# Optimization experiments

Hardware: AMD Instinct MI355X
Metric: run time of the kernel (lower is better)

## Reference

```python
import jax, jax.numpy as jnp
import numpy as np

B, T, D, H = 2, 512, 512, 8
HD = D // H
FF = 4 * D
MOM_BETA, NOV_BETA, NOV_GAIN = 0.9, 0.95, 3.0
LR_MIN, LR_MAX, MAX_FW_NORM = 0.5, 3.0, 32.0


def setup_inputs() -> dict:
    key = jax.random.key(0)
    ks = jax.random.split(key, 10)
    s = 1.0 / np.sqrt(D)
    return {
        'x': jax.random.normal(ks[0], (B, T, D), jnp.float32),
        'Wq': jax.random.normal(ks[1], (D, D), jnp.float32) * s,
        'Wk1': jax.random.normal(ks[2], (D, D), jnp.float32) * s,
        'Wk2': jax.random.normal(ks[3], (D, D), jnp.float32) * s,
        'Wv': jax.random.normal(ks[4], (D, D), jnp.float32) * s,
        'Wo': jax.random.normal(ks[5], (D, D), jnp.float32) * s,
        'lambda_logit': jnp.zeros((H,), jnp.float32),  # sigmoid -> lambda_init = 0.5
        'ln1_g': jnp.ones((D,), jnp.float32), 'ln1_b': jnp.zeros((D,), jnp.float32),
        'base_weight': jax.random.normal(ks[6], (D, D), jnp.float32) * s,  # ~xavier
        'ttt_bias': jnp.zeros((D,), jnp.float32),
        'log_inner_lr': jnp.log(jnp.asarray(0.05, jnp.float32)),
        'ln2_g': jnp.ones((D,), jnp.float32), 'ln2_b': jnp.zeros((D,), jnp.float32),
        'W1': jax.random.normal(ks[7], (FF, D), jnp.float32) * s,
        'b1': jnp.zeros((FF,), jnp.float32),
        'W2': jax.random.normal(ks[8], (D, FF), jnp.float32) * (1.0 / np.sqrt(FF)),
        'b2': jnp.zeros((D,), jnp.float32),
        'ln3_g': jnp.ones((D,), jnp.float32), 'ln3_b': jnp.zeros((D,), jnp.float32),
    }


def _ln(x, g, b):
    m = x.mean(-1, keepdims=True)
    v = jnp.mean((x - m) ** 2, -1, keepdims=True)
    return (x - m) / jnp.sqrt(v + 1e-5) * g + b


def _diff_attn(x, Wq, Wk1, Wk2, Wv, Wo, lambda_logit):
    b, t, d = x.shape
    def heads(w):
        return jnp.einsum('btd,od->bto', x, w).reshape(b, t, H, HD).transpose(0, 2, 1, 3)
    q, k1, k2, v = heads(Wq), heads(Wk1), heads(Wk2), heads(Wv)
    scale = HD ** -0.5
    s1 = jnp.einsum('bhqd,bhkd->bhqk', q, k1) * scale
    s2 = jnp.einsum('bhqd,bhkd->bhqk', q, k2) * scale
    mask = jnp.tril(jnp.ones((t, t), bool))
    neg = jnp.finfo(s1.dtype).min
    s1 = jnp.where(mask, s1, neg)
    s2 = jnp.where(mask, s2, neg)
    lam = jax.nn.sigmoid(lambda_logit)[None, :, None, None]
    attn = jax.nn.softmax(s1, -1) - lam * jax.nn.softmax(s2, -1)
    attn = attn / jnp.clip(jnp.abs(attn).sum(-1, keepdims=True), 1e-6, None)
    o = jnp.einsum('bhqk,bhkd->bhqd', attn, v).transpose(0, 2, 1, 3).reshape(b, t, d)
    return jnp.einsum('btd,od->bto', o, Wo)


def _ttt(x, base_weight, ttt_bias, log_inner_lr):
    b = x.shape[0]
    inner_lr = jnp.clip(jnp.exp(log_inner_lr), 1e-5, 1.0)
    fw0 = jnp.broadcast_to(base_weight, (b, D, D)).astype(x.dtype) + 0.0
    mom0 = jnp.zeros_like(fw0)
    ema0 = jnp.zeros((b, D), x.dtype)
    lrm0 = jnp.ones((b, 1), x.dtype)

    def step(carry, x_t):  # x_t: [B, D]
        fw, mom, ema, lrm = carry
        y = jnp.einsum('bij,bj->bi', fw, x_t) + ttt_bias
        err = (y - x_t) / float(D)  # targets=None -> target is x_t
        g = jax.lax.stop_gradient(err[:, :, None] * x_t[:, None, :])  # first_order
        mom2 = MOM_BETA * mom + (1.0 - MOM_BETA) * g
        nov = jnp.abs(x_t - ema).mean(-1, keepdims=True)  # [B, 1]
        lr_scale = jnp.clip(1.0 + NOV_GAIN * nov, LR_MIN, LR_MAX)
        lrm2 = NOV_BETA * lrm + (1.0 - NOV_BETA) * lr_scale
        ema2 = NOV_BETA * ema + (1.0 - NOV_BETA) * x_t
        fw2 = fw - (inner_lr * lrm2)[:, :, None] * mom2
        norm = jnp.clip(jnp.sqrt((fw2 * fw2).sum((1, 2), keepdims=True)), 1e-6, None)
        fw2 = fw2 * jnp.minimum(MAX_FW_NORM / norm, 1.0)
        return (fw2, mom2, ema2, lrm2), y

    _, ys = jax.lax.scan(step, (fw0, mom0, ema0, lrm0), x.transpose(1, 0, 2))
    return ys.transpose(1, 0, 2)


def reference(x, Wq, Wk1, Wk2, Wv, Wo, lambda_logit, ln1_g, ln1_b, base_weight, ttt_bias, log_inner_lr, ln2_g, ln2_b, W1, b1, W2, b2, ln3_g, ln3_b):
    h = x + _diff_attn(_ln(x, ln1_g, ln1_b), Wq, Wk1, Wk2, Wv, Wo, lambda_logit)
    h = h + _ttt(_ln(h, ln2_g, ln2_b), base_weight, ttt_bias, log_inner_lr)
    z = _ln(h, ln3_g, ln3_b)
    z = jax.nn.gelu(jnp.einsum('btd,fd->btf', z, W1) + b1, approximate=False)
    h = h + jnp.einsum('btf,df->btd', z, W2) + b2
    return h
```

## Files before the change

### kernel.cpp

```cpp
#include <hip/hip_runtime.h>
#include <hip/hip_fp16.h>

typedef _Float16 f16;
typedef f16 f16x4 __attribute__((ext_vector_type(4)));
typedef f16 f16x8 __attribute__((ext_vector_type(8)));
typedef float f32x4 __attribute__((ext_vector_type(4)));
typedef unsigned uint2v __attribute__((ext_vector_type(2)));

#define DEVI static __device__ __forceinline__

DEVI void gload_lds16(const void* g, void* l) {
  __builtin_amdgcn_global_load_lds(
      (const __attribute__((address_space(1))) unsigned int*)g,
      (__attribute__((address_space(3))) unsigned int*)l, 16, 0, 0);
}

DEVI float wave_red_sum64(float v) {
#pragma unroll
  for (int m = 1; m < 64; m <<= 1) v += __shfl_xor(v, m, 64);
  return v;
}
DEVI float wave_red_max64(float v) {
#pragma unroll
  for (int m = 1; m < 64; m <<= 1) v = fmaxf(v, __shfl_xor(v, m, 64));
  return v;
}

template <int CTRL>
DEVI float dpp_addf(float v) {
  int s = __builtin_amdgcn_update_dpp(0, __float_as_int(v), CTRL, 0xF, 0xF, true);
  return v + __int_as_float(s);
}
DEVI float xor16_add(float v) {
#if __has_builtin(__builtin_amdgcn_permlane16_swap)
  uint2v r = __builtin_amdgcn_permlane16_swap(__float_as_uint(v), __float_as_uint(v), false, false);
  return __uint_as_float(r.x) + __uint_as_float(r.y);
#else
  int s = __builtin_amdgcn_ds_swizzle(__float_as_int(v), 0x401F);
  return v + __int_as_float(s);
#endif
}
DEVI float xor32_add(float v) {
#if __has_builtin(__builtin_amdgcn_permlane32_swap)
  uint2v r = __builtin_amdgcn_permlane32_swap(__float_as_uint(v), __float_as_uint(v), false, false);
  return __uint_as_float(r.x) + __uint_as_float(r.y);
#else
  int s = __builtin_amdgcn_ds_bpermute(((threadIdx.x & 63) ^ 32) << 2, __float_as_int(v));
  return v + __int_as_float(s);
#endif
}
DEVI float allred64(float v) {
  v = dpp_addf<0xB1>(v);
  v = dpp_addf<0x4E>(v);
  v = dpp_addf<0x141>(v);
  v = dpp_addf<0x140>(v);
  v = xor16_add(v);
  return xor32_add(v);
}
DEVI float red16g(float v) {
  v = dpp_addf<0xB1>(v);
  v = dpp_addf<0x4E>(v);
  v = dpp_addf<0x141>(v);
  v = dpp_addf<0x140>(v);
  return v;
}

__global__ void cvt_all_kernel(const float* __restrict__ s0, const float* __restrict__ s1,
                               const float* __restrict__ s2, const float* __restrict__ s3,
                               const float* __restrict__ s4, const float* __restrict__ s5,
                               const float* __restrict__ s6, f16* __restrict__ d) {
  const int blk = blockIdx.x;
  const float* s; long dofs; int local;
  if (blk < 256)       { s = s0; dofs = 0;       local = blk; }
  else if (blk < 512)  { s = s1; dofs = 262144;  local = blk - 256; }
  else if (blk < 768)  { s = s2; dofs = 524288;  local = blk - 512; }
  else if (blk < 1024) { s = s3; dofs = 786432;  local = blk - 768; }
  else if (blk < 1280) { s = s4; dofs = 1048576; local = blk - 1024; }
  else if (blk < 2304) { s = s5; dofs = 1310720; local = blk - 1280; }
  else                 { s = s6; dofs = 2359296; local = blk - 2304; }
  const long i = (long)local * 1024 + threadIdx.x * 4;
  float4 v = *(const float4*)(s + i);
  f16x4 o = {(f16)v.x, (f16)v.y, (f16)v.z, (f16)v.w};
  *(f16x4*)(d + dofs + i) = o;
}

__global__ void ln_kernel(const float* __restrict__ in, const float* __restrict__ add,
                          const float* __restrict__ g, const float* __restrict__ b,
                          float* __restrict__ sumout, float* __restrict__ lnf,
                          f16* __restrict__ lnh) {
  const int row = blockIdx.x * 4 + (threadIdx.x >> 6);
  const int lane = threadIdx.x & 63;
  const long base = (long)row * 512;
  const int c0 = lane * 4, c1 = 256 + lane * 4;
  float4 a0 = *(const float4*)(in + base + c0);
  float4 a1 = *(const float4*)(in + base + c1);
  if (add) {
    float4 d0 = *(const float4*)(add + base + c0);
    float4 d1 = *(const float4*)(add + base + c1);
    a0.x += d0.x; a0.y += d0.y; a0.z += d0.z; a0.w += d0.w;
    a1.x += d1.x; a1.y += d1.y; a1.z += d1.z; a1.w += d1.w;
  }
  if (sumout) {
    *(float4*)(sumout + base + c0) = a0;
    *(float4*)(sumout + base + c1) = a1;
  }
  float v[8] = {a0.x, a0.y, a0.z, a0.w, a1.x, a1.y, a1.z, a1.w};
  float s = 0.f;
#pragma unroll
  for (int k = 0; k < 8; k++) s += v[k];
  s = wave_red_sum64(s);
  const float mean = s * (1.f / 512.f);
  float vs = 0.f;
#pragma unroll
  for (int k = 0; k < 8; k++) { float d = v[k] - mean; vs += d * d; }
  vs = wave_red_sum64(vs);
  const float rstd = rsqrtf(vs * (1.f / 512.f) + 1e-5f);
  float4 g0 = *(const float4*)(g + c0), g1 = *(const float4*)(g + c1);
  float4 p0 = *(const float4*)(b + c0), p1 = *(const float4*)(b + c1);
  const float gg[8] = {g0.x, g0.y, g0.z, g0.w, g1.x, g1.y, g1.z, g1.w};
  const float bv[8] = {p0.x, p0.y, p0.z, p0.w, p1.x, p1.y, p1.z, p1.w};
  float y[8];
#pragma unroll
  for (int k = 0; k < 8; k++) y[k] = (v[k] - mean) * rstd * gg[k] + bv[k];
  if (lnf) {
    float4 o0 = {y[0], y[1], y[2], y[3]}, o1 = {y[4], y[5], y[6], y[7]};
    *(float4*)(lnf + base + c0) = o0;
    *(float4*)(lnf + base + c1) = o1;
  }
  if (lnh) {
    f16x4 o0 = {(f16)y[0], (f16)y[1], (f16)y[2], (f16)y[3]};
    f16x4 o1 = {(f16)y[4], (f16)y[5], (f16)y[6], (f16)y[7]};
    *(f16x4*)(lnh + base + c0) = o0;
    *(f16x4*)(lnh + base + c1) = o1;
  }
}

enum { EPI_QKV = 0, EPI_SCORES = 2, EPI_PV = 3, EPI_WO = 4, EPI_GELU = 5, EPI_OUT = 6 };

template <int EPI>
__launch_bounds__(256, 1) __global__
void gemm_bt(const f16* __restrict__ A, const f16* __restrict__ W, int lda, int ldw,
             long Az, long Wz, void* __restrict__ dst, const float* __restrict__ bias,
             const float* __restrict__ resid, int K, float scale, int zofs, int hcp) {
  if (EPI == EPI_SCORES && blockIdx.x > blockIdx.y) return;
  __shared__ f16 lA[128 * 64];
  __shared__ f16 lB[128 * 64];
  const int tid = threadIdx.x;
  const int wave = tid >> 6, lane = tid & 63;
  const int z = blockIdx.z;
  const f16* Ab;
  const f16* Wb;
  if (EPI == EPI_SCORES) {
    const int v_ = (z >= hcp) ? 1 : 0, head = z - v_ * hcp;
    Ab = A + (long)head * 32768 + (long)blockIdx.y * 128 * lda;
    Wb = W + (long)v_ * 524288 + (long)head * 32768 + (long)blockIdx.x * 128 * ldw;
  } else {
    Ab = A + (long)z * Az + (long)blockIdx.y * 128 * lda;
    Wb = W + (long)z * Wz + (long)blockIdx.x * 128 * ldw;
  }

  f32x4 acc[4][4];
#pragma unroll
  for (int a = 0; a < 4; a++)
#pragma unroll
    for (int q = 0; q < 4; q++) acc[a][q] = (f32x4){0.f, 0.f, 0.f, 0.f};

  int srow[4], scol[4];
#pragma unroll
  for (int i = 0; i < 4; i++) {
    int c = i * 256 + tid;
    int row = c >> 3;
    int colb = (c & 7) << 4;
    srow[i] = row;
    scol[i] = (colb ^ ((row & 7) << 4)) >> 1;
  }

  for (int k0 = 0; k0 < K; k0 += 64) {
    __syncthreads();
#pragma unroll
    for (int i = 0; i < 4; i++) {
      const int le = (i * 256 + wave * 64) * 8;
      gload_lds16(Ab + (long)srow[i] * lda + k0 + scol[i], lA + le);
      gload_lds16(Wb + (long)srow[i] * ldw + k0 + scol[i], lB + le);
    }
    __syncthreads();
    const int wm = (wave >> 1) * 64, wn = (wave & 1) * 64;
#pragma unroll
    for (int km = 0; km < 2; km++) {
      const int kb = km * 64 + ((lane >> 4) << 4);
      f16x8 af[4], bfv[4];
#pragma unroll
      for (int mf = 0; mf < 4; mf++) {
        int r = wm + mf * 16 + (lane & 15);
        af[mf] = *(const f16x8*)((const char*)lA + r * 128 + (kb ^ ((r & 7) << 4)));
      }
#pragma unroll
      for (int nf = 0; nf < 4; nf++) {
        int r = wn + nf * 16 + (lane & 15);
        bfv[nf] = *(const f16x8*)((const char*)lB + r * 128 + (kb ^ ((r & 7) << 4)));
      }
#pragma unroll
      for (int mf = 0; mf < 4; mf++)
#pragma unroll
        for (int nf = 0; nf < 4; nf++)
          acc[mf][nf] = __builtin_amdgcn_mfma_f32_16x16x32_f16(af[mf], bfv[nf], acc[mf][nf], 0, 0, 0);
    }
  }

  const int wm = (wave >> 1) * 64, wn = (wave & 1) * 64;
  const int rbase = blockIdx.y * 128 + wm + ((lane >> 4) << 2);
  const int cbase = blockIdx.x * 128 + wn + (lane & 15);
#pragma unroll
  for (int mf = 0; mf < 4; mf++)
#pragma unroll
    for (int nf = 0; nf < 4; nf++)
#pragma unroll
      for (int j = 0; j < 4; j++) {
        const int m = rbase + mf * 16 + j;
        const int n = cbase + nf * 16;
        const float v = acc[mf][nf][j];
        if (EPI == EPI_QKV) {
          f16* d = (f16*)dst + (long)z * 524288;
          if (z < 3)
            d[(long)((m >> 9) * 8 + (n >> 6)) * 32768 + (m & 511) * 64 + (n & 63)] = (f16)v;
          else
            d[(long)((m >> 9) * 8 + (n >> 6)) * 32768 + (n & 63) * 512 + (m & 511)] = (f16)v;
        } else if (EPI == EPI_SCORES) {
          ((float*)dst)[(long)z * 262144 + (long)m * 512 + n] = v * scale;
        } else if (EPI == EPI_PV) {
          if (n < 64) {
            const int hh = z + zofs;
            ((f16*)dst)[(long)((hh >> 3) * 512 + m) * 512 + (hh & 7) * 64 + n] = (f16)v;
          }
        } else if (EPI == EPI_WO) {
          ((float*)dst)[(long)m * 512 + n] = v + resid[(long)m * 512 + n];
        } else if (EPI == EPI_GELU) {
          const float u = v + bias[n];
          ((f16*)dst)[(long)m * 2048 + n] = (f16)(0.5f * u * (1.f + erff(u * 0.70710678118f)));
        } else {
          ((float*)dst)[(long)m * 512 + n] = v + bias[n] + resid[(long)m * 512 + n];
        }
      }
}

__global__ void softmax_diff_kernel(const float* __restrict__ S1, const float* __restrict__ S2,
                                    const float* __restrict__ lamlog, f16* __restrict__ attn,
                                    int zofs) {
  const int rid = blockIdx.x * 4 + (threadIdx.x >> 6);
  const int lane = threadIdx.x & 63;
  const int z = rid >> 9, i = rid & 511;
  const float lam = 1.f / (1.f + __expf(-lamlog[(z + zofs) & 7]));
  const long base = (long)z * 262144 + (long)i * 512;
  const int c0 = lane * 4, c1 = 256 + lane * 4;
  float4 xa = *(const float4*)(S1 + base + c0);
  float4 xb = *(const float4*)(S1 + base + c1);
  float4 ya = *(const float4*)(S2 + base + c0);
  float4 yb = *(const float4*)(S2 + base + c1);
  float s1v[8] = {xa.x, xa.y, xa.z, xa.w, xb.x, xb.y, xb.z, xb.w};
  float s2v[8] = {ya.x, ya.y, ya.z, ya.w, yb.x, yb.y, yb.z, yb.w};
  int cols[8];
#pragma unroll
  for (int k = 0; k < 8; k++) cols[k] = (k < 4) ? (c0 + k) : (c1 + k - 4);
  float m1 = -3.0e38f, m2 = -3.0e38f;
#pragma unroll
  for (int k = 0; k < 8; k++)
    if (cols[k] <= i) { m1 = fmaxf(m1, s1v[k]); m2 = fmaxf(m2, s2v[k]); }
  m1 = wave_red_max64(m1);
  m2 = wave_red_max64(m2);
  float z1 = 0.f, z2 = 0.f, e1[8], e2[8];
#pragma unroll
  for (int k = 0; k < 8; k++) {
    const bool valid = cols[k] <= i;
    e1[k] = valid ? __expf(s1v[k] - m1) : 0.f;
    e2[k] = valid ? __expf(s2v[k] - m2) : 0.f;
    z1 += e1[k]; z2 += e2[k];
  }
  z1 = wave_red_sum64(z1);
  z2 = wave_red_sum64(z2);
  const float r1 = 1.f / z1, r2 = lam / z2;
  float p[8], l1 = 0.f;
#pragma unroll
  for (int k = 0; k < 8; k++) { p[k] = e1[k] * r1 - e2[k] * r2; l1 += fabsf(p[k]); }
  l1 = wave_red_sum64(l1);
  const float rn = 1.f / fmaxf(l1, 1e-6f);
  f16x4 o0 = {(f16)(p[0] * rn), (f16)(p[1] * rn), (f16)(p[2] * rn), (f16)(p[3] * rn)};
  f16x4 o1 = {(f16)(p[4] * rn), (f16)(p[5] * rn), (f16)(p[6] * rn), (f16)(p[7] * rn)};
  *(f16x4*)(attn + base + c0) = o0;
  *(f16x4*)(attn + base + c1) = o1;
}

#define ALD4(dst, p) asm volatile("global_load_dwordx4 %0, %1, off" : "=&v"(dst) : "v"(p) : "memory")
#define ALD1(dst, p) asm volatile("global_load_dword %0, %1, off" : "=&v"(dst) : "v"(p) : "memory")
#define VMWAIT(N)                                                             \
  {                                                                           \
    asm volatile("s_waitcnt vmcnt(" #N ")" ::: "memory");                     \
    __builtin_amdgcn_sched_barrier(0);                                        \
  }

#define EISSUE(X)                                                             \
  {                                                                           \
    ALD1(X[0], pe);        ALD1(X[1], pe + 512);                              \
    ALD1(X[2], pe + 1024); ALD1(X[3], pe + 1536);                             \
    ALD1(X[4], pe + 2048); ALD1(X[5], pe + 2560);                             \
    ALD1(X[6], pe + 3072); ALD1(X[7], pe + 3584);                             \
    pe += 4096;                                                               \
  }
#define ESTEP(V, T)                                                           \
  {                                                                           \
    dp[(long)(T) * 512] = fabsf((V) - ema);                                   \
    ema = fmaf(0.95f, ema, 0.05f * (V));                                      \
  }

__launch_bounds__(64, 1) __global__
void eta_diff_kernel(const float* __restrict__ x2, float* __restrict__ diff) {
  const int blk = blockIdx.x;
  const int b = blk >> 3;
  const int col = (blk & 7) * 64 + threadIdx.x;
  const float* pe = x2 + (long)b * 262144 + col;
  float* dp = diff + (long)b * 262144 + col;
  float ema = 0.f;
  float EA[8], EB[8];
  EISSUE(EA);
  EISSUE(EB);
  VMWAIT(8);
#pragma unroll 1
  for (int t = 0; t < 512; t += 16) {
    ESTEP(EA[0], t + 0); ESTEP(EA[1], t + 1); ESTEP(EA[2], t + 2); ESTEP(EA[3], t + 3);
    ESTEP(EA[4], t + 4); ESTEP(EA[5], t + 5); ESTEP(EA[6], t + 6); ESTEP(EA[7], t + 7);
    EISSUE(EA);
    VMWAIT(16);
    ESTEP(EB[0], t + 8);  ESTEP(EB[1], t + 9);  ESTEP(EB[2], t + 10); ESTEP(EB[3], t + 11);
    ESTEP(EB[4], t + 12); ESTEP(EB[5], t + 13); ESTEP(EB[6], t + 14); ESTEP(EB[7], t + 15);
    EISSUE(EB);
    VMWAIT(16);
  }
  asm volatile("s_waitcnt vmcnt(0)" ::: "memory");
}

__global__ void eta_nov_kernel(const float* __restrict__ diff, float* __restrict__ nov) {
  const int row = blockIdx.x * 4 + (threadIdx.x >> 6);
  const int lane = threadIdx.x & 63;
  const float* dp = diff + (long)row * 512 + lane * 4;
  float4 a0 = *(const float4*)dp;
  float4 a1 = *(const float4*)(dp + 256);
  float s = ((a0.x + a0.y) + (a0.z + a0.w)) + ((a1.x + a1.y) + (a1.z + a1.w));
  s = wave_red_sum64(s);
  if (lane == 0) nov[row] = s * (1.f / 512.f);
}

__global__ void eta_scan_kernel(const float* __restrict__ nov, const float* __restrict__ loglr,
                                float* __restrict__ eta) {
  if (threadIdx.x != 0) return;
  const int b = blockIdx.x;
  float ilr = expf(loglr[0]);
  ilr = fminf(fmaxf(ilr, 1e-5f), 1.f);
  float lrm = 1.f;
  const float* pb = nov + (long)b * 512;
#pragma unroll 8
  for (int t = 0; t < 512; t++) {
    const float ls = fminf(fmaxf(fmaf(3.f, pb[t], 1.f), 0.5f), 3.f);
    lrm = fmaf(0.95f, lrm, 0.05f * ls);
    eta[b * 512 + t] = ilr * lrm;
  }
}

#define TISSUE(X, XR, ET)                                                     \
  {                                                                           \
    ALD4(X[0], pxc);        ALD4(X[1], pxc + 4);                              \
    ALD4(X[2], pxc + 512);  ALD4(X[3], pxc + 516);                            \
    ALD4(X[4], pxc + 1024); ALD4(X[5], pxc + 1028);                           \
    ALD4(X[6], pxc + 1536); ALD4(X[7], pxc + 1540);                           \
    ALD1(XR[0], pxr);        ALD1(XR[1], pxr + 512);                          \
    ALD1(XR[2], pxr + 1024); ALD1(XR[3], pxr + 1536);                         \
    ALD4(ET, per);                                                            \
    pxc += 2048; pxr += 2048; per += 4;                                       \
  }

#define TSTEP(X0, X1, XRv, EV, T)                                             \
  {                                                                           \
    float a0_ = fw[0] * X0.x, a1_ = fw[1] * X0.y;                             \
    float a2_ = fw[2] * X0.z, a3_ = fw[3] * X0.w;                             \
    a0_ = fmaf(fw[4], X1.x, a0_); a1_ = fmaf(fw[5], X1.y, a1_);               \
    a2_ = fmaf(fw[6], X1.z, a2_); a3_ = fmaf(fw[7], X1.w, a3_);               \
    float p_ = (a0_ + a1_) + (a2_ + a3_);                                     \
    p_ = allred64(p_);                                                        \
    const float y_ = p_ + biasr;                                              \
    if (lane == 0) ys[ysofs + (long)(T) * 512] = y_;                          \
    const float c1_ = (y_ - (XRv)) * (0.1f / 512.f);                          \
    const float e_ = (EV);                                                    \
    const float xv_[8] = {X0.x, X0.y, X0.z, X0.w, X1.x, X1.y, X1.z, X1.w};    \
    float n0_ = 0.f, n1_ = 0.f, n2_ = 0.f, n3_ = 0.f;                         \
    _Pragma("unroll")                                                         \
    for (int i_ = 0; i_ < 2; i_++) {                                          \
      mom[4*i_+0] = fmaf(0.9f, mom[4*i_+0], c1_ * xv_[4*i_+0]);               \
      fw[4*i_+0] = fmaf(-e_, mom[4*i_+0], fw[4*i_+0]);                        \
      n0_ = fmaf(fw[4*i_+0], fw[4*i_+0], n0_);                                \
      mom[4*i_+1] = fmaf(0.9f, mom[4*i_+1], c1_ * xv_[4*i_+1]);               \
      fw[4*i_+1] = fmaf(-e_, mom[4*i_+1], fw[4*i_+1]);                        \
      n1_ = fmaf(fw[4*i_+1], fw[4*i_+1], n1_);                                \
      mom[4*i_+2] = fmaf(0.9f, mom[4*i_+2], c1_ * xv_[4*i_+2]);               \
      fw[4*i_+2] = fmaf(-e_, mom[4*i_+2], fw[4*i_+2]);                        \
      n2_ = fmaf(fw[4*i_+2], fw[4*i_+2], n2_);                                \
      mom[4*i_+3] = fmaf(0.9f, mom[4*i_+3], c1_ * xv_[4*i_+3]);               \
      fw[4*i_+3] = fmaf(-e_, mom[4*i_+3], fw[4*i_+3]);                        \
      n3_ = fmaf(fw[4*i_+3], fw[4*i_+3], n3_);                                \
    }                                                                         \
    float nsq_ = (n0_ + n1_) + (n2_ + n3_);                                   \
    nsq_ = red16g(nsq_);                                                      \
    if ((lane & 15) == 0)                                                     \
      normpart[(((long)(T)) * 1024 + blk) * 4 + (lane >> 4)] = nsq_;          \
  }

__launch_bounds__(64, 1) __global__
void ttt_fast_kernel(const float* __restrict__ x2, const float* __restrict__ base_w,
                     const float* __restrict__ tbias, const float* __restrict__ eta,
                     float* __restrict__ ys, float* __restrict__ normpart) {
  const int blk = blockIdx.x;
  const int b = blk >> 9;
  const int row = blk & 511;
  const int lane = threadIdx.x;
  const float* xb = x2 + (long)b * 262144;
  const float* er = eta + b * 512;
  const long ysofs = (long)b * 262144 + row;

  float fw[8], mom[8];
  {
    const float* bp = base_w + (long)row * 512 + lane * 8;
    float4 f0 = *(const float4*)bp, f1 = *(const float4*)(bp + 4);
    fw[0] = f0.x; fw[1] = f0.y; fw[2] = f0.z; fw[3] = f0.w;
    fw[4] = f1.x; fw[5] = f1.y; fw[6] = f1.z; fw[7] = f1.w;
  }
#pragma unroll
  for (int i = 0; i < 8; i++) mom[i] = 0.f;
  const float biasr = tbias[row];

  const float* pxc = xb + lane * 8;
  const float* pxr = xb + row;
  const float* per = er;

  f32x4 XA[8], XB[8], EA, EB;
  float RA[4], RB[4];
  TISSUE(XA, RA, EA);
  TISSUE(XB, RB, EB);
  VMWAIT(13);

#pragma unroll 1
  for (int T = 0; T < 512; T += 8) {
    TSTEP(XA[0], XA[1], RA[0], EA.x, T + 0);
    TSTEP(XA[2], XA[3], RA[1], EA.y, T + 1);
    TSTEP(XA[4], XA[5], RA[2], EA.z, T + 2);
    TSTEP(XA[6], XA[7], RA[3], EA.w, T + 3);
    TISSUE(XA, RA, EA);
    VMWAIT(21);
    TSTEP(XB[0], XB[1], RB[0], EB.x, T + 4);
    TSTEP(XB[2], XB[3], RB[1], EB.y, T + 5);
    TSTEP(XB[4], XB[5], RB[2], EB.z, T + 6);
    TSTEP(XB[6], XB[7], RB[3], EB.w, T + 7);
    TISSUE(XB, RB, EB);
    VMWAIT(21);
  }
  asm volatile("s_waitcnt vmcnt(0)" ::: "memory");
}

__global__ void verify_kernel(const float* __restrict__ normpart, int* __restrict__ flag) {
  const int t = blockIdx.x;
  const int tid = threadIdx.x;
  const int wave = tid >> 6, lane = tid & 63;
  float4 v = *(const float4*)(normpart + (((long)t * 1024) + tid) * 4);
  float s = (v.x + v.y) + (v.z + v.w);
  s = wave_red_sum64(s);
  __shared__ float part[16];
  if (lane == 0) part[wave] = s;
  __syncthreads();
  if (tid == 0) {
    float s0 = 0.f, s1 = 0.f;
#pragma unroll
    for (int w = 0; w < 8; w++) { s0 += part[w]; s1 += part[8 + w]; }
    if (s0 > 1020.f || s1 > 1020.f) atomicOr(flag, 1);
  }
}

__launch_bounds__(1024, 1) __global__
void ttt_fallback_kernel(const int* __restrict__ flag, const float* __restrict__ x2,
                         const float* __restrict__ base_w, const float* __restrict__ tbias,
                         const float* __restrict__ eta, float* __restrict__ ys,
                         float* __restrict__ fwg, float* __restrict__ momg) {
  if (flag[0] == 0) return;
  const int b = blockIdx.x;
  const int tid = threadIdx.x;
  const int wave = tid >> 6, lane = tid & 63;
  float* fw = fwg + (long)b * 262144;
  float* mm = momg + (long)b * 262144;
  for (int e = tid; e < 262144; e += 1024) { fw[e] = base_w[e]; mm[e] = 0.f; }
  __shared__ float xs[512], errs[512], red[16];
  const float* xb = x2 + (long)b * 262144;
  for (int t = 0; t < 512; t++) {
    __syncthreads();
    if (tid < 512) xs[tid] = xb[t * 512 + tid];
    __syncthreads();
    if (tid < 512) {
      float acc = 0.f;
      for (int c = 0; c < 512; c++) acc = fmaf(fw[(long)tid * 512 + c], xs[c], acc);
      const float y = acc + tbias[tid];
      ys[((long)b * 512 + t) * 512 + tid] = y;
      errs[tid] = (y - xs[tid]) * (1.f / 512.f);
    }
    __syncthreads();
    const float eta_t = eta[b * 512 + t];
    float nsq = 0.f;
    for (int e = tid; e < 262144; e += 1024) {
      const int r = e >> 9, c = e & 511;
      const float m2 = fmaf(0.9f, mm[e], 0.1f * errs[r] * xs[c]);
      mm[e] = m2;
      const float f2 = fmaf(-eta_t, m2, fw[e]);
      fw[e] = f2;
      nsq = fmaf(f2, f2, nsq);
    }
    nsq = wave_red_sum64(nsq);
    if (lane == 0) red[wave] = nsq;
    __syncthreads();
    if (tid == 0) {
      float s = 0.f;
      for (int w = 0; w < 16; w++) s += red[w];
      red[0] = s;
    }
    __syncthreads();
    const float norm = fmaxf(sqrtf(red[0]), 1e-6f);
    const float sc = fminf(32.f / norm, 1.f);
    if (sc < 1.f)
      for (int e = tid; e < 262144; e += 1024) fw[e] *= sc;
  }
}

extern "C" void kernel_launch(void* const* d_in, const int* in_sizes, int n_in,
                              void* d_out, int out_size, void* d_ws, size_t ws_size,
                              hipStream_t stream) {
  (void)in_sizes; (void)n_in; (void)out_size;
  const float* x      = (const float*)d_in[0];
  const float* Wq     = (const float*)d_in[1];
  const float* Wk1    = (const float*)d_in[2];
  const float* Wk2    = (const float*)d_in[3];
  const float* Wv     = (const float*)d_in[4];
  const float* Wo     = (const float*)d_in[5];
  const float* lamlog = (const float*)d_in[6];
  const float* ln1g   = (const float*)d_in[7];
  const float* ln1b   = (const float*)d_in[8];
  const float* basew  = (const float*)d_in[9];
  const float* tttb   = (const float*)d_in[10];
  const float* loglr  = (const float*)d_in[11];
  const float* ln2g   = (const float*)d_in[12];
  const float* ln2b   = (const float*)d_in[13];
  const float* W1     = (const float*)d_in[14];
  const float* b1     = (const float*)d_in[15];
  const float* W2     = (const float*)d_in[16];
  const float* b2     = (const float*)d_in[17];
  const float* ln3g   = (const float*)d_in[18];
  const float* ln3b   = (const float*)d_in[19];
  float* out = (float*)d_out;

  char* ws = (char*)d_ws;
  size_t off = 0;
  auto alloc = [&](size_t bytes) {
    size_t o = off;
    off += (bytes + 255) & ~(size_t)255;
    return o;
  };
  f16* WqH   = (f16*)(ws + alloc(262144 * 2));
  f16* Wk1H  = (f16*)(ws + alloc(262144 * 2));
  f16* Wk2H  = (f16*)(ws + alloc(262144 * 2));
  f16* WvH   = (f16*)(ws + alloc(262144 * 2));
  f16* WoH   = (f16*)(ws + alloc(262144 * 2));
  f16* W1H   = (f16*)(ws + alloc(1048576 * 2));
  f16* W2H   = (f16*)(ws + alloc(1048576 * 2));
  (void)Wk1H; (void)Wk2H; (void)WvH; (void)W1H;
  f16* xlnH  = (f16*)(ws + alloc(524288 * 2));
  f16* qh    = (f16*)(ws + alloc(524288 * 2));
  f16* k1h   = (f16*)(ws + alloc(524288 * 2));
  f16* k2h   = (f16*)(ws + alloc(524288 * 2));
  f16* vTh   = (f16*)(ws + alloc(524288 * 2));
  (void)k2h;
  f16* obtd  = (f16*)(ws + alloc(524288 * 2));
  f16* x3h   = (f16*)(ws + alloc(524288 * 2));
  f16* zh    = (f16*)(ws + alloc(2097152 * 2));
  float* h1  = (float*)(ws + alloc(524288 * 4));
  float* x2  = (float*)(ws + alloc(524288 * 4));
  float* ysb = (float*)(ws + alloc(524288 * 4));
  float* h2  = (float*)(ws + alloc(524288 * 4));
  float* eta = (float*)(ws + alloc(1024 * 4));
  float* npt = (float*)(ws + alloc((size_t)512 * 1024 * 4 * 4));
  float* nvd = (float*)(ws + alloc(524288 * 4));
  float* nov = (float*)(ws + alloc(1024 * 4));
  int* flag  = (int*)(ws + alloc(256));
  float* fwfb  = (float*)(ws + alloc(524288 * 4));
  float* momfb = (float*)(ws + alloc(524288 * 4));

  int hc = 16;
  while (hc > 1 && off + (size_t)hc * (262144ull * 4 * 2 + 262144ull * 2) > ws_size) hc >>= 1;
  float* S1  = (float*)(ws + alloc((size_t)hc * 262144 * 4));
  float* S2  = (float*)(ws + alloc((size_t)hc * 262144 * 4));
  f16* attnb = (f16*)(ws + alloc((size_t)hc * 262144 * 2));
  (void)S2;

  cvt_all_kernel<<<3328, 256, 0, stream>>>(Wq, Wk1, Wk2, Wv, Wo, W1, W2, WqH);

  ln_kernel<<<256, 256, 0, stream>>>(x, nullptr, ln1g, ln1b, nullptr, nullptr, xlnH);

  gemm_bt<EPI_QKV><<<dim3(4, 8, 4), 256, 0, stream>>>(
      xlnH, WqH, 512, 512, 0, 262144, qh, nullptr, nullptr, 512, 1.f, 0, 0);

  const int nc = 16 / hc;
  for (int c = 0; c < nc; c++) {
    const int cs = c * hc;
    gemm_bt<EPI_SCORES><<<dim3(4, 4, 2 * hc), 256, 0, stream>>>(
        qh + (long)cs * 32768, k1h + (long)cs * 32768, 64, 64, 0, 0, S1,
        nullptr, nullptr, 64, 0.125f, 0, hc);
    softmax_diff_kernel<<<hc * 128, 256, 0, stream>>>(S1, S2, lamlog, attnb, cs);
    gemm_bt<EPI_PV><<<dim3(1, 4, hc), 256, 0, stream>>>(
        attnb, vTh + (long)cs * 32768, 512, 512, 262144, 32768, obtd,
        nullptr, nullptr, 512, 1.f, cs, 0);
  }

  gemm_bt<EPI_WO><<<dim3(4, 8, 1), 256, 0, stream>>>(obtd, WoH, 512, 512, 0, 0, h1, nullptr, x, 512, 1.f, 0, 0);

  ln_kernel<<<256, 256, 0, stream>>>(h1, nullptr, ln2g, ln2b, nullptr, x2, nullptr);

  hipMemsetAsync(flag, 0, 4, stream);
  eta_diff_kernel<<<16, 64, 0, stream>>>(x2, nvd);
  eta_nov_kernel<<<256, 256, 0, stream>>>(nvd, nov);
  eta_scan_kernel<<<2, 64, 0, stream>>>(nov, loglr, eta);
  ttt_fast_kernel<<<1024, 64, 0, stream>>>(x2, basew, tttb, eta, ysb, npt);
  verify_kernel<<<512, 1024, 0, stream>>>(npt, flag);
  ttt_fallback_kernel<<<2, 1024, 0, stream>>>(flag, x2, basew, tttb, eta, ysb, fwfb, momfb);

  ln_kernel<<<256, 256, 0, stream>>>(h1, ysb, ln3g, ln3b, h2, nullptr, x3h);

  gemm_bt<EPI_GELU><<<dim3(16, 8, 1), 256, 0, stream>>>(x3h, W1H, 512, 512, 0, 0, zh, b1, nullptr, 512, 1.f, 0, 0);
  gemm_bt<EPI_OUT><<<dim3(4, 8, 1), 256, 0, stream>>>(zh, W2H, 2048, 2048, 0, 0, out, b2, h2, 2048, 1.f, 0, 0);
}
```

Measured before the change: 313.0 us.

## Process two fast-weight rows per wave and batch outputs through a transpose

Each single-wave TTT block now owns two rows of the fast weight instead of one, which halves the block count and shares the streamed x loads across both rows. Per-step y values and norm partials are buffered in registers and written as float4 chunks every 8 steps into a time-contiguous layout. A new transpose kernel then restores the layout that the following kernels expect. The aim is to cut the scattered per-step scalar stores and the redundant x traffic, at the cost of more registers, an extra launch and fewer blocks to spread across the CUs.

```diff
diff --git a/kernel.cpp b/kernel.cpp
--- a/kernel.cpp
+++ b/kernel.cpp
@@ -56,13 +56,6 @@
   v = dpp_addf<0x140>(v);
   v = xor16_add(v);
   return xor32_add(v);
-}
-DEVI float red16g(float v) {
-  v = dpp_addf<0xB1>(v);
-  v = dpp_addf<0x4E>(v);
-  v = dpp_addf<0x141>(v);
-  v = dpp_addf<0x140>(v);
-  return v;
 }
 
 __global__ void cvt_all_kernel(const float* __restrict__ s0, const float* __restrict__ s1,
@@ -364,118 +357,151 @@
   }
 }
 
-#define TISSUE(X, XR, ET)                                                     \
+DEVI float dot8(const f32x4 F0, const f32x4 F1, const f32x4 X0, const f32x4 X1) {
+  float a0 = F0.x * X0.x, a1 = F0.y * X0.y, a2 = F0.z * X0.z, a3 = F0.w * X0.w;
+  a0 = fmaf(F1.x, X1.x, a0); a1 = fmaf(F1.y, X1.y, a1);
+  a2 = fmaf(F1.z, X1.z, a2); a3 = fmaf(F1.w, X1.w, a3);
+  return (a0 + a1) + (a2 + a3);
+}
+DEVI void upd8(f32x4& M0, f32x4& M1, f32x4& F0, f32x4& F1, float c1, float e,
+               const f32x4 X0, const f32x4 X1, float& ns) {
+  M0.x = fmaf(0.9f, M0.x, c1 * X0.x); F0.x = fmaf(-e, M0.x, F0.x); ns = fmaf(F0.x, F0.x, ns);
+  M0.y = fmaf(0.9f, M0.y, c1 * X0.y); F0.y = fmaf(-e, M0.y, F0.y); ns = fmaf(F0.y, F0.y, ns);
+  M0.z = fmaf(0.9f, M0.z, c1 * X0.z); F0.z = fmaf(-e, M0.z, F0.z); ns = fmaf(F0.z, F0.z, ns);
+  M0.w = fmaf(0.9f, M0.w, c1 * X0.w); F0.w = fmaf(-e, M0.w, F0.w); ns = fmaf(F0.w, F0.w, ns);
+  M1.x = fmaf(0.9f, M1.x, c1 * X1.x); F1.x = fmaf(-e, M1.x, F1.x); ns = fmaf(F1.x, F1.x, ns);
+  M1.y = fmaf(0.9f, M1.y, c1 * X1.y); F1.y = fmaf(-e, M1.y, F1.y); ns = fmaf(F1.y, F1.y, ns);
+  M1.z = fmaf(0.9f, M1.z, c1 * X1.z); F1.z = fmaf(-e, M1.z, F1.z); ns = fmaf(F1.z, F1.z, ns);
+  M1.w = fmaf(0.9f, M1.w, c1 * X1.w); F1.w = fmaf(-e, M1.w, F1.w); ns = fmaf(F1.w, F1.w, ns);
+}
+
+#define TISSUE2(X, RA, RB, ET)                                                \
   {                                                                           \
     ALD4(X[0], pxc);        ALD4(X[1], pxc + 4);                              \
     ALD4(X[2], pxc + 512);  ALD4(X[3], pxc + 516);                            \
     ALD4(X[4], pxc + 1024); ALD4(X[5], pxc + 1028);                           \
     ALD4(X[6], pxc + 1536); ALD4(X[7], pxc + 1540);                           \
-    ALD1(XR[0], pxr);        ALD1(XR[1], pxr + 512);                          \
-    ALD1(XR[2], pxr + 1024); ALD1(XR[3], pxr + 1536);                         \
+    ALD1(RA[0], pxra);        ALD1(RA[1], pxra + 512);                        \
+    ALD1(RA[2], pxra + 1024); ALD1(RA[3], pxra + 1536);                       \
+    ALD1(RB[0], pxrb);        ALD1(RB[1], pxrb + 512);                        \
+    ALD1(RB[2], pxrb + 1024); ALD1(RB[3], pxrb + 1536);                       \
     ALD4(ET, per);                                                            \
-    pxc += 2048; pxr += 2048; per += 4;                                       \
-  }
-
-#define TSTEP(X0, X1, XRv, EV, T)                                             \
+    pxc += 2048; pxra += 2048; pxrb += 2048; per += 4;                        \
+  }
+
+#define TSTEP2(X0v, X1v, rAv, rBv, ev, K)                                     \
   {                                                                           \
-    float a0_ = fw[0] * X0.x, a1_ = fw[1] * X0.y;                             \
-    float a2_ = fw[2] * X0.z, a3_ = fw[3] * X0.w;                             \
-    a0_ = fmaf(fw[4], X1.x, a0_); a1_ = fmaf(fw[5], X1.y, a1_);               \
-    a2_ = fmaf(fw[6], X1.z, a2_); a3_ = fmaf(fw[7], X1.w, a3_);               \
-    float p_ = (a0_ + a1_) + (a2_ + a3_);                                     \
-    p_ = allred64(p_);                                                        \
-    const float y_ = p_ + biasr;                                              \
-    if (lane == 0) ys[ysofs + (long)(T) * 512] = y_;                          \
-    const float c1_ = (y_ - (XRv)) * (0.1f / 512.f);                          \
-    const float e_ = (EV);                                                    \
-    const float xv_[8] = {X0.x, X0.y, X0.z, X0.w, X1.x, X1.y, X1.z, X1.w};    \
-    float n0_ = 0.f, n1_ = 0.f, n2_ = 0.f, n3_ = 0.f;                         \
-    _Pragma("unroll")                                                         \
-    for (int i_ = 0; i_ < 2; i_++) {                                          \
-      mom[4*i_+0] = fmaf(0.9f, mom[4*i_+0], c1_ * xv_[4*i_+0]);               \
-      fw[4*i_+0] = fmaf(-e_, mom[4*i_+0], fw[4*i_+0]);                        \
-      n0_ = fmaf(fw[4*i_+0], fw[4*i_+0], n0_);                                \
-      mom[4*i_+1] = fmaf(0.9f, mom[4*i_+1], c1_ * xv_[4*i_+1]);               \
-      fw[4*i_+1] = fmaf(-e_, mom[4*i_+1], fw[4*i_+1]);                        \
-      n1_ = fmaf(fw[4*i_+1], fw[4*i_+1], n1_);                                \
-      mom[4*i_+2] = fmaf(0.9f, mom[4*i_+2], c1_ * xv_[4*i_+2]);               \
-      fw[4*i_+2] = fmaf(-e_, mom[4*i_+2], fw[4*i_+2]);                        \
-      n2_ = fmaf(fw[4*i_+2], fw[4*i_+2], n2_);                                \
-      mom[4*i_+3] = fmaf(0.9f, mom[4*i_+3], c1_ * xv_[4*i_+3]);               \
-      fw[4*i_+3] = fmaf(-e_, mom[4*i_+3], fw[4*i_+3]);                        \
-      n3_ = fmaf(fw[4*i_+3], fw[4*i_+3], n3_);                                \
-    }                                                                         \
-    float nsq_ = (n0_ + n1_) + (n2_ + n3_);                                   \
-    nsq_ = red16g(nsq_);                                                      \
-    if ((lane & 15) == 0)                                                     \
-      normpart[(((long)(T)) * 1024 + blk) * 4 + (lane >> 4)] = nsq_;          \
+    const float pA_ = allred64(dot8(fA0, fA1, X0v, X1v));                     \
+    const float pB_ = allred64(dot8(fB0, fB1, X0v, X1v));                     \
+    const float yA_ = pA_ + biasA, yB_ = pB_ + biasB;                         \
+    ysA[K] = yA_; ysB[K] = yB_;                                               \
+    const float c1A_ = (yA_ - (rAv)) * (0.1f / 512.f);                        \
+    const float c1B_ = (yB_ - (rBv)) * (0.1f / 512.f);                        \
+    const float e_ = (ev);                                                    \
+    float ns_ = 0.f;                                                          \
+    upd8(mA0, mA1, fA0, fA1, c1A_, e_, X0v, X1v, ns_);                        \
+    upd8(mB0, mB1, fB0, fB1, c1B_, e_, X0v, X1v, ns_);                        \
+    np8[K] = allred64(ns_);                                                   \
   }
 
 __launch_bounds__(64, 1) __global__
 void ttt_fast_kernel(const float* __restrict__ x2, const float* __restrict__ base_w,
                      const float* __restrict__ tbias, const float* __restrict__ eta,
-                     float* __restrict__ ys, float* __restrict__ normpart) {
+                     float* __restrict__ yT, float* __restrict__ npT) {
   const int blk = blockIdx.x;
-  const int b = blk >> 9;
-  const int row = blk & 511;
+  const int b = blk >> 8;
+  const int rA = blk & 255;
   const int lane = threadIdx.x;
   const float* xb = x2 + (long)b * 262144;
-  const float* er = eta + b * 512;
-  const long ysofs = (long)b * 262144 + row;
-
-  float fw[8], mom[8];
-  {
-    const float* bp = base_w + (long)row * 512 + lane * 8;
-    float4 f0 = *(const float4*)bp, f1 = *(const float4*)(bp + 4);
-    fw[0] = f0.x; fw[1] = f0.y; fw[2] = f0.z; fw[3] = f0.w;
-    fw[4] = f1.x; fw[5] = f1.y; fw[6] = f1.z; fw[7] = f1.w;
-  }
-#pragma unroll
-  for (int i = 0; i < 8; i++) mom[i] = 0.f;
-  const float biasr = tbias[row];
+
+  f32x4 fA0, fA1, fB0, fB1;
+  float biasA, biasB;
+  ALD4(fA0, base_w + (long)rA * 512 + lane * 8);
+  ALD4(fA1, base_w + (long)rA * 512 + lane * 8 + 4);
+  ALD4(fB0, base_w + (long)(rA + 256) * 512 + lane * 8);
+  ALD4(fB1, base_w + (long)(rA + 256) * 512 + lane * 8 + 4);
+  ALD1(biasA, tbias + rA);
+  ALD1(biasB, tbias + rA + 256);
+
+  f32x4 mA0 = {0.f, 0.f, 0.f, 0.f}, mA1 = mA0, mB0 = mA0, mB1 = mA0;
+  float ysA[8], ysB[8], np8[8];
 
   const float* pxc = xb + lane * 8;
-  const float* pxr = xb + row;
-  const float* per = er;
+  const float* pxra = xb + rA;
+  const float* pxrb = xb + rA + 256;
+  const float* per = eta + b * 512;
+  float* pyA = yT + (long)(b * 512 + rA) * 512;
+  float* pyB = yT + (long)(b * 512 + rA + 256) * 512;
+  float* pnp = npT + (long)blk * 512;
 
   f32x4 XA[8], XB[8], EA, EB;
-  float RA[4], RB[4];
-  TISSUE(XA, RA, EA);
-  TISSUE(XB, RB, EB);
-  VMWAIT(13);
+  float RA0[4], RB0[4], RA1[4], RB1[4];
+  TISSUE2(XA, RA0, RB0, EA);
+  TISSUE2(XB, RA1, RB1, EB);
+  VMWAIT(17);
 
 #pragma unroll 1
   for (int T = 0; T < 512; T += 8) {
-    TSTEP(XA[0], XA[1], RA[0], EA.x, T + 0);
-    TSTEP(XA[2], XA[3], RA[1], EA.y, T + 1);
-    TSTEP(XA[4], XA[5], RA[2], EA.z, T + 2);
-    TSTEP(XA[6], XA[7], RA[3], EA.w, T + 3);
-    TISSUE(XA, RA, EA);
-    VMWAIT(21);
-    TSTEP(XB[0], XB[1], RB[0], EB.x, T + 4);
-    TSTEP(XB[2], XB[3], RB[1], EB.y, T + 5);
-    TSTEP(XB[4], XB[5], RB[2], EB.z, T + 6);
-    TSTEP(XB[6], XB[7], RB[3], EB.w, T + 7);
-    TISSUE(XB, RB, EB);
-    VMWAIT(21);
+    TSTEP2(XA[0], XA[1], RA0[0], RB0[0], EA.x, 0);
+    TSTEP2(XA[2], XA[3], RA0[1], RB0[1], EA.y, 1);
+    TSTEP2(XA[4], XA[5], RA0[2], RB0[2], EA.z, 2);
+    TSTEP2(XA[6], XA[7], RA0[3], RB0[3], EA.w, 3);
+    TISSUE2(XA, RA0, RB0, EA);
+    VMWAIT(17);
+    TSTEP2(XB[0], XB[1], RA1[0], RB1[0], EB.x, 4);
+    TSTEP2(XB[2], XB[3], RA1[1], RB1[1], EB.y, 5);
+    TSTEP2(XB[4], XB[5], RA1[2], RB1[2], EB.z, 6);
+    TSTEP2(XB[6], XB[7], RA1[3], RB1[3], EB.w, 7);
+    if (lane == 0) {
+      *(float4*)(pyA + T)     = (float4){ysA[0], ysA[1], ysA[2], ysA[3]};
+      *(float4*)(pyA + T + 4) = (float4){ysA[4], ysA[5], ysA[6], ysA[7]};
+      *(float4*)(pyB + T)     = (float4){ysB[0], ysB[1], ysB[2], ysB[3]};
+      *(float4*)(pyB + T + 4) = (float4){ysB[4], ysB[5], ysB[6], ysB[7]};
+      *(float4*)(pnp + T)     = (float4){np8[0], np8[1], np8[2], np8[3]};
+      *(float4*)(pnp + T + 4) = (float4){np8[4], np8[5], np8[6], np8[7]};
+    }
+    TISSUE2(XB, RA1, RB1, EB);
+    VMWAIT(23);
   }
   asm volatile("s_waitcnt vmcnt(0)" ::: "memory");
 }
 
-__global__ void verify_kernel(const float* __restrict__ normpart, int* __restrict__ flag) {
+__global__ void transpose3_kernel(const float* __restrict__ yT, const float* __restrict__ npT,
+                                  float* __restrict__ ysb, float* __restrict__ npv) {
+  __shared__ float tile[64][65];
+  const int s = blockIdx.z;
+  const float* src = (s < 2) ? (yT + (long)s * 262144) : npT;
+  float* dst = (s < 2) ? (ysb + (long)s * 262144) : npv;
+  const int ti = blockIdx.y, tj = blockIdx.x;
+  const int tr = threadIdx.x >> 4;
+  const int tc = (threadIdx.x & 15) * 4;
+#pragma unroll
+  for (int p = 0; p < 4; p++) {
+    const int r = tr + p * 16;
+    float4 v = *(const float4*)(src + (long)(ti * 64 + r) * 512 + tj * 64 + tc);
+    tile[r][tc] = v.x; tile[r][tc + 1] = v.y; tile[r][tc + 2] = v.z; tile[r][tc + 3] = v.w;
+  }
+  __syncthreads();
+#pragma unroll
+  for (int p = 0; p < 4; p++) {
+    const int j = tr + p * 16;
+    float4 v = {tile[tc][j], tile[tc + 1][j], tile[tc + 2][j], tile[tc + 3][j]};
+    *(float4*)(dst + (long)(tj * 64 + j) * 512 + ti * 64 + tc) = v;
+  }
+}
+
+__global__ void verify_kernel(const float* __restrict__ npv, int* __restrict__ flag) {
   const int t = blockIdx.x;
   const int tid = threadIdx.x;
   const int wave = tid >> 6, lane = tid & 63;
-  float4 v = *(const float4*)(normpart + (((long)t * 1024) + tid) * 4);
-  float s = (v.x + v.y) + (v.z + v.w);
+  float s = npv[(long)t * 512 + tid];
   s = wave_red_sum64(s);
-  __shared__ float part[16];
+  __shared__ float part[8];
   if (lane == 0) part[wave] = s;
   __syncthreads();
   if (tid == 0) {
-    float s0 = 0.f, s1 = 0.f;
-#pragma unroll
-    for (int w = 0; w < 8; w++) { s0 += part[w]; s1 += part[8 + w]; }
+    const float s0 = (part[0] + part[1]) + (part[2] + part[3]);
+    const float s1 = (part[4] + part[5]) + (part[6] + part[7]);
     if (s0 > 1020.f || s1 > 1020.f) atomicOr(flag, 1);
   }
 }
@@ -587,7 +613,9 @@
   float* ysb = (float*)(ws + alloc(524288 * 4));
   float* h2  = (float*)(ws + alloc(524288 * 4));
   float* eta = (float*)(ws + alloc(1024 * 4));
-  float* npt = (float*)(ws + alloc((size_t)512 * 1024 * 4 * 4));
+  float* yT  = (float*)(ws + alloc(524288 * 4));
+  float* npT = (float*)(ws + alloc(262144 * 4));
+  float* npv = (float*)(ws + alloc(262144 * 4));
   float* nvd = (float*)(ws + alloc(524288 * 4));
   float* nov = (float*)(ws + alloc(1024 * 4));
   int* flag  = (int*)(ws + alloc(256));
@@ -628,8 +656,9 @@
   eta_diff_kernel<<<16, 64, 0, stream>>>(x2, nvd);
   eta_nov_kernel<<<256, 256, 0, stream>>>(nvd, nov);
   eta_scan_kernel<<<2, 64, 0, stream>>>(nov, loglr, eta);
-  ttt_fast_kernel<<<1024, 64, 0, stream>>>(x2, basew, tttb, eta, ysb, npt);
-  verify_kernel<<<512, 1024, 0, stream>>>(npt, flag);
+  ttt_fast_kernel<<<512, 64, 0, stream>>>(x2, basew, tttb, eta, yT, npT);
+  transpose3_kernel<<<dim3(8, 8, 3), 256, 0, stream>>>(yT, npT, ysb, npv);
+  verify_kernel<<<512, 512, 0, stream>>>(npv, flag);
   ttt_fallback_kernel<<<2, 1024, 0, stream>>>(flag, x2, basew, tttb, eta, ysb, fwfb, momfb);
 
   ln_kernel<<<256, 256, 0, stream>>>(h1, ysb, ln3g, ln3b, h2, nullptr, x3h);
```

Result: no change. 314.2 us (+0.4%).
